# Kernel tuning notes

Hardware: AMD Instinct MI355X
Metric: run time of the kernel (lower is better)

Reference implementation:

```python
import jax, jax.numpy as jnp
import numpy as np

B, T, IN, H, OUT = 4096, 365, 32, 256, 1


def setup_inputs() -> dict:
    key = jax.random.key(0)
    ks = jax.random.split(key, 6)
    s_ih = 1.0 / np.sqrt(H)
    return {
        "xd": jax.random.normal(ks[0], (B, T, IN), dtype=jnp.float32),
        "w_ih": jax.random.uniform(ks[1], (4 * H, IN), minval=-s_ih, maxval=s_ih, dtype=jnp.float32),
        "w_hh": jax.random.uniform(ks[2], (4 * H, H), minval=-s_ih, maxval=s_ih, dtype=jnp.float32),
        "b": jax.random.uniform(ks[3], (4 * H,), minval=-s_ih, maxval=s_ih, dtype=jnp.float32),
        "w_out": jax.random.uniform(ks[4], (OUT, H), minval=-s_ih, maxval=s_ih, dtype=jnp.float32),
        "b_out": jax.random.uniform(ks[5], (OUT,), minval=-s_ih, maxval=s_ih, dtype=jnp.float32),
    }


def reference(xd, w_ih, w_hh, b, w_out, b_out):
    # xd: [B, T, IN]. Scan LSTM cell over time; gate order i, f, g, o (equinox/torch).
    Bsz = xd.shape[0]
    Hs = w_hh.shape[1]
    xs = jnp.swapaxes(xd, 0, 1)  # [T, B, IN]
    # Precompute input projections for all timesteps (same math, one big GEMM).
    x_proj = jnp.einsum("tbi,gi->tbg", xs, w_ih) + b  # [T, B, 4H]

    def step(state, xp):
        h, c = state  # [B, H] each
        gates = xp + h @ w_hh.T  # [B, 4H]
        i, f, g, o = jnp.split(gates, 4, axis=-1)
        i = jax.nn.sigmoid(i)
        f = jax.nn.sigmoid(f)
        g = jnp.tanh(g)
        o = jax.nn.sigmoid(o)
        c = f * c + i * g
        h = o * jnp.tanh(c)
        return (h, c), None

    init = (jnp.zeros((Bsz, Hs), xd.dtype), jnp.zeros((Bsz, Hs), xd.dtype))
    (h_T, _), _ = jax.lax.scan(step, init, x_proj)
    return jax.nn.relu(h_T @ w_out.T + b_out)  # [B, OUT]
```

## Files before the change

kernel.cpp:

```cpp
#include <hip/hip_runtime.h>
#include <hip/hip_fp16.h>

#define T_SZ 365
#define IN_SZ 32
#define H_SZ 256
#define G4 1024
#define K_SZ 288
#define M_BLK 32
#define NGRP 128
#define NTHR 512
#define NBLK 256
#define XPB 80
#define HROWB 512
#define HS_BYTES (M_BLK * HROWB)

#define ARR_OFF (640*1024)
#define HX_OFF  (1024*1024)

typedef _Float16 f16x8 __attribute__((ext_vector_type(8)));
typedef _Float16 f16x2 __attribute__((ext_vector_type(2)));
typedef float f32x4 __attribute__((ext_vector_type(4)));
typedef unsigned long long u64;

__device__ __forceinline__ float fast_sigmoid(float x) {
    float e = __builtin_amdgcn_exp2f(-1.4426950408889634f * x);
    return __builtin_amdgcn_rcpf(1.0f + e);
}
__device__ __forceinline__ float fast_tanh(float x) {
    float e = __builtin_amdgcn_exp2f(2.8853900817779268f * x);
    return 1.0f - 2.0f * __builtin_amdgcn_rcpf(1.0f + e);
}

__global__ void pack_w_kernel(const float* __restrict__ w_ih,
                              const float* __restrict__ w_hh,
                              _Float16* __restrict__ wp) {
    int idx = blockIdx.x * 256 + threadIdx.x;
    if (idx >= G4 * K_SZ) return;
    int g = idx / K_SZ, k = idx - g * K_SZ;
    float v = (k < H_SZ) ? w_hh[g * H_SZ + k] : w_ih[g * IN_SZ + (k - H_SZ)];
    wp[idx] = (_Float16)v;
}

__global__ void init_sync_kernel(unsigned int* arrive) {
    for (int i = threadIdx.x; i < NGRP * 2 * 16; i += 256) arrive[i] = 0u;
}

__global__ __launch_bounds__(NTHR, 2) void lstm_kernel(
    const float* __restrict__ xd, const float* __restrict__ b,
    const _Float16* __restrict__ wp, const float* __restrict__ w_out,
    const float* __restrict__ b_out, float* __restrict__ out,
    u64* hx, unsigned int* arrive)
{
    __shared__ __align__(16) char hsb[2 * HS_BYTES];
    __shared__ __align__(16) char x_s[M_BLK * XPB];

    const int tid  = threadIdx.x;
    const int wq   = tid >> 6;
    const int lane = tid & 63;
    const int quad = lane >> 4;
    const int l16  = lane & 15;
    const int blk  = blockIdx.x;
    const int g    = blk & (NGRP - 1);
    const int q    = blk >> 7;

    const int jcol = q * 128 + wq * 16 + l16;

    f16x8 wfr[4][9];
#pragma unroll
    for (int G = 0; G < 4; ++G) {
        const _Float16* wr = wp + (size_t)(G * 256 + jcol) * K_SZ + quad * 8;
#pragma unroll
        for (int kt = 0; kt < 9; ++kt)
            wfr[G][kt] = *(const f16x8*)(wr + kt * 32);
    }
    float bias[4];
#pragma unroll
    for (int G = 0; G < 4; ++G) bias[G] = b[G * 256 + jcol];

    const int swz_l = (l16 & 7) << 4;
    int a_off[8];
#pragma unroll
    for (int kt = 0; kt < 8; ++kt)
        a_off[kt] = l16 * HROWB + ((kt * 64 + quad * 16) ^ swz_l);
    const int x_off = l16 * XPB + quad * 16;

    const int xr = tid >> 4;
    const int xe = tid & 15;
    const int xs_byte = xr * XPB + xe * 4;
    const float* xrow = xd + (size_t)(g * M_BLK + xr) * (T_SZ * IN_SZ) + xe * 2;
    float2 xa = *(const float2*)xrow;

    const int pr  = tid >> 5;
    const int pw  = tid & 31;
    const int swz_p = (pr & 7) << 4;
    const int push_l0 = pr * HROWB + ((q * 256 + pw * 8) ^ swz_p);
    const int pull_l0 = pr * HROWB + (((1 - q) * 256 + pw * 8) ^ swz_p);
    const int push_u0 = q * 1024 + tid;
    const int pull_u0 = (1 - q) * 1024 + tid;

    {
        u64* z = (u64*)hsb;
#pragma unroll
        for (int i = 0; i < 4; ++i) z[tid * 4 + i] = 0ull;
    }
    *(f16x2*)(x_s + xs_byte) = (f16x2){(_Float16)xa.x, (_Float16)xa.y};

    f32x4 creg[2];
    creg[0] = (f32x4){0.f, 0.f, 0.f, 0.f};
    creg[1] = (f32x4){0.f, 0.f, 0.f, 0.f};

    __syncthreads();

    unsigned int* myf = &arrive[(g * 2 + q) * 16];
    unsigned int* prf = &arrive[(g * 2 + (1 - q)) * 16];
    const f32x4 vzero = {0.f, 0.f, 0.f, 0.f};

    int pb = 0;
    for (int t = 0; t < T_SZ; ++t) {
        const char* hsR = hsb + pb * HS_BYTES;
        char* hsW = hsb + (pb ^ 1) * HS_BYTES;

        f32x4 acc[2][4];
#pragma unroll
        for (int mt = 0; mt < 2; ++mt)
#pragma unroll
            for (int G = 0; G < 4; ++G) acc[mt][G] = vzero;

#pragma unroll
        for (int kt = 0; kt < 8; ++kt) {
            f16x8 a0 = *(const f16x8*)(hsR + a_off[kt]);
            f16x8 a1 = *(const f16x8*)(hsR + a_off[kt] + 16 * HROWB);
#pragma unroll
            for (int G = 0; G < 4; ++G) {
                acc[0][G] = __builtin_amdgcn_mfma_f32_16x16x32_f16(a0, wfr[G][kt], acc[0][G], 0, 0, 0);
                acc[1][G] = __builtin_amdgcn_mfma_f32_16x16x32_f16(a1, wfr[G][kt], acc[1][G], 0, 0, 0);
            }
        }
        {
            f16x8 a0 = *(const f16x8*)(x_s + x_off);
            f16x8 a1 = *(const f16x8*)(x_s + x_off + 16 * XPB);
#pragma unroll
            for (int G = 0; G < 4; ++G) {
                acc[0][G] = __builtin_amdgcn_mfma_f32_16x16x32_f16(a0, wfr[G][8], acc[0][G], 0, 0, 0);
                acc[1][G] = __builtin_amdgcn_mfma_f32_16x16x32_f16(a1, wfr[G][8], acc[1][G], 0, 0, 0);
            }
        }

#pragma unroll
        for (int mt = 0; mt < 2; ++mt) {
#pragma unroll
            for (int r = 0; r < 4; ++r) {
                float iv = fast_sigmoid(acc[mt][0][r] + bias[0]);
                float fv = fast_sigmoid(acc[mt][1][r] + bias[1]);
                float gv = fast_tanh  (acc[mt][2][r] + bias[2]);
                float ov = fast_sigmoid(acc[mt][3][r] + bias[3]);
                float cv = fv * creg[mt][r] + iv * gv;
                creg[mt][r] = cv;
                float hv = ov * fast_tanh(cv);
                int m = mt * 16 + quad * 4 + r;
                *(_Float16*)(hsW + m * HROWB + ((jcol * 2) ^ ((m & 7) << 4))) = (_Float16)hv;
            }
        }
        asm volatile("s_waitcnt lgkmcnt(0)" ::: "memory");
        __builtin_amdgcn_s_barrier();

        u64* hxg = hx + ((size_t)pb * NGRP + g) * 2048;
        {
            u64 p0 = *(const u64*)(hsW + push_l0);
            u64 p1 = *(const u64*)(hsW + push_l0 + 16 * HROWB);
            __hip_atomic_store(&hxg[push_u0],       p0, __ATOMIC_RELAXED, __HIP_MEMORY_SCOPE_AGENT);
            __hip_atomic_store(&hxg[push_u0 + 512], p1, __ATOMIC_RELAXED, __HIP_MEMORY_SCOPE_AGENT);
        }
        if (t + 1 < T_SZ) {
            xa = *(const float2*)(xrow + (size_t)(t + 1) * IN_SZ);
            asm volatile("s_waitcnt vmcnt(1)" ::: "memory");
        } else {
            asm volatile("s_waitcnt vmcnt(0)" ::: "memory");
        }
        __builtin_amdgcn_s_barrier();

        if (tid == 0) {
            __hip_atomic_store(myf, (unsigned int)(t + 1),
                               __ATOMIC_RELAXED, __HIP_MEMORY_SCOPE_AGENT);
            while (__hip_atomic_load(prf, __ATOMIC_RELAXED, __HIP_MEMORY_SCOPE_AGENT) < (unsigned int)(t + 1))
                __builtin_amdgcn_s_sleep(1);
        }
        __builtin_amdgcn_s_barrier();
        asm volatile("" ::: "memory");

        {
            u64 v0 = __hip_atomic_load(&hxg[pull_u0],       __ATOMIC_RELAXED, __HIP_MEMORY_SCOPE_AGENT);
            u64 v1 = __hip_atomic_load(&hxg[pull_u0 + 512], __ATOMIC_RELAXED, __HIP_MEMORY_SCOPE_AGENT);
            *(u64*)(hsW + pull_l0)              = v0;
            *(u64*)(hsW + pull_l0 + 16 * HROWB) = v1;
        }
        if (t + 1 < T_SZ)
            *(f16x2*)(x_s + xs_byte) = (f16x2){(_Float16)xa.x, (_Float16)xa.y};
        asm volatile("s_waitcnt lgkmcnt(0)" ::: "memory");
        __builtin_amdgcn_s_barrier();
        pb ^= 1;
    }

    if (q == 0) {
        const char* hsF = hsb + pb * HS_BYTES;
        const int m = tid >> 4, p = tid & 15;
        const int swzm = (m & 7) << 4;
        float sum = 0.f;
#pragma unroll
        for (int jj = 0; jj < 16; ++jj) {
            int j = p * 16 + jj;
            sum += (float)*(const _Float16*)(hsF + m * HROWB + ((j * 2) ^ swzm)) * w_out[j];
        }
        sum += __shfl_xor(sum, 1);
        sum += __shfl_xor(sum, 2);
        sum += __shfl_xor(sum, 4);
        sum += __shfl_xor(sum, 8);
        if (p == 0) out[(size_t)g * M_BLK + m] = fmaxf(sum + b_out[0], 0.f);
    }
}

extern "C" void kernel_launch(void* const* d_in, const int* in_sizes, int n_in,
                              void* d_out, int out_size, void* d_ws, size_t ws_size,
                              hipStream_t stream) {
    const float* xd    = (const float*)d_in[0];
    const float* w_ih  = (const float*)d_in[1];
    const float* w_hh  = (const float*)d_in[2];
    const float* b     = (const float*)d_in[3];
    const float* w_out = (const float*)d_in[4];
    const float* b_out = (const float*)d_in[5];
    float* out = (float*)d_out;

    _Float16* wp = (_Float16*)d_ws;
    unsigned int* arrive = (unsigned int*)((char*)d_ws + ARR_OFF);
    u64* hx = (u64*)((char*)d_ws + HX_OFF);

    pack_w_kernel<<<(G4 * K_SZ + 255) / 256, 256, 0, stream>>>(w_ih, w_hh, wp);
    init_sync_kernel<<<1, 256, 0, stream>>>(arrive);
    lstm_kernel<<<NBLK, NTHR, 0, stream>>>(xd, b, wp, w_out, b_out, out, hx, arrive);
}
```

Baseline: 1.608 ms.

## Overlap cross-block h exchange with local-half recurrent GEMM via split-K pipelining

Splits the recurrent K dimension into the block's own hidden half and the partner block's half. The own-half MFMAs (plus the x-projection tile) for the next step are issued before and after the inter-block flag wait, and the partner's h values stay in registers until the next step. This hides spin-wait and global-load latency behind tensor work and drops one barrier per step. It also prefetches x two steps ahead, at the cost of more live registers and more complex hand-written waitcnt ordering.

```diff
diff --git a/kernel.cpp b/kernel.cpp
--- a/kernel.cpp
+++ b/kernel.cpp
@@ -45,6 +45,19 @@
     for (int i = threadIdx.x; i < NGRP * 2 * 16; i += 256) arrive[i] = 0u;
 }
 
+#define GEMM_TILE(base, off, stride, slot) do {                                            \
+    f16x8 a0_ = *(const f16x8*)((const char*)(base) + (off));                              \
+    f16x8 a1_ = *(const f16x8*)((const char*)(base) + (off) + 16 * (stride));              \
+    acc[0][0] = __builtin_amdgcn_mfma_f32_16x16x32_f16(a0_, wfr[0][slot], acc[0][0],0,0,0);\
+    acc[1][0] = __builtin_amdgcn_mfma_f32_16x16x32_f16(a1_, wfr[0][slot], acc[1][0],0,0,0);\
+    acc[0][1] = __builtin_amdgcn_mfma_f32_16x16x32_f16(a0_, wfr[1][slot], acc[0][1],0,0,0);\
+    acc[1][1] = __builtin_amdgcn_mfma_f32_16x16x32_f16(a1_, wfr[1][slot], acc[1][1],0,0,0);\
+    acc[0][2] = __builtin_amdgcn_mfma_f32_16x16x32_f16(a0_, wfr[2][slot], acc[0][2],0,0,0);\
+    acc[1][2] = __builtin_amdgcn_mfma_f32_16x16x32_f16(a1_, wfr[2][slot], acc[1][2],0,0,0);\
+    acc[0][3] = __builtin_amdgcn_mfma_f32_16x16x32_f16(a0_, wfr[3][slot], acc[0][3],0,0,0);\
+    acc[1][3] = __builtin_amdgcn_mfma_f32_16x16x32_f16(a1_, wfr[3][slot], acc[1][3],0,0,0);\
+} while (0)
+
 __global__ __launch_bounds__(NTHR, 2) void lstm_kernel(
     const float* __restrict__ xd, const float* __restrict__ b,
     const _Float16* __restrict__ wp, const float* __restrict__ w_out,
@@ -64,6 +77,8 @@
     const int q    = blk >> 7;
 
     const int jcol = q * 128 + wq * 16 + l16;
+    const int ktO  = q * 4;
+    const int ktP  = (1 - q) * 4;
 
     f16x8 wfr[4][9];
 #pragma unroll
@@ -88,7 +103,6 @@
     const int xe = tid & 15;
     const int xs_byte = xr * XPB + xe * 4;
     const float* xrow = xd + (size_t)(g * M_BLK + xr) * (T_SZ * IN_SZ) + xe * 2;
-    float2 xa = *(const float2*)xrow;
 
     const int pr  = tid >> 5;
     const int pw  = tid & 31;
@@ -103,7 +117,11 @@
 #pragma unroll
         for (int i = 0; i < 4; ++i) z[tid * 4 + i] = 0ull;
     }
-    *(f16x2*)(x_s + xs_byte) = (f16x2){(_Float16)xa.x, (_Float16)xa.y};
+    {
+        float2 x0 = *(const float2*)xrow;
+        *(f16x2*)(x_s + xs_byte) = (f16x2){(_Float16)x0.x, (_Float16)x0.y};
+    }
+    float2 xa = *(const float2*)(xrow + IN_SZ);
 
     f32x4 creg[2];
     creg[0] = (f32x4){0.f, 0.f, 0.f, 0.f};
@@ -115,36 +133,34 @@
     unsigned int* prf = &arrive[(g * 2 + (1 - q)) * 16];
     const f32x4 vzero = {0.f, 0.f, 0.f, 0.f};
 
+    f32x4 acc[2][4];
+#pragma unroll
+    for (int mt = 0; mt < 2; ++mt)
+#pragma unroll
+        for (int G = 0; G < 4; ++G) acc[mt][G] = vzero;
+    GEMM_TILE(x_s, x_off, XPB, 8);
+#pragma unroll
+    for (int kt = 0; kt < 4; ++kt)
+        GEMM_TILE(hsb, a_off[ktO + kt], HROWB, ktO + kt);
+
+    u64 pv0 = 0, pv1 = 0;
     int pb = 0;
     for (int t = 0; t < T_SZ; ++t) {
-        const char* hsR = hsb + pb * HS_BYTES;
-        char* hsW = hsb + (pb ^ 1) * HS_BYTES;
-
-        f32x4 acc[2][4];
-#pragma unroll
-        for (int mt = 0; mt < 2; ++mt)
-#pragma unroll
-            for (int G = 0; G < 4; ++G) acc[mt][G] = vzero;
-
-#pragma unroll
-        for (int kt = 0; kt < 8; ++kt) {
-            f16x8 a0 = *(const f16x8*)(hsR + a_off[kt]);
-            f16x8 a1 = *(const f16x8*)(hsR + a_off[kt] + 16 * HROWB);
-#pragma unroll
-            for (int G = 0; G < 4; ++G) {
-                acc[0][G] = __builtin_amdgcn_mfma_f32_16x16x32_f16(a0, wfr[G][kt], acc[0][G], 0, 0, 0);
-                acc[1][G] = __builtin_amdgcn_mfma_f32_16x16x32_f16(a1, wfr[G][kt], acc[1][G], 0, 0, 0);
-            }
-        }
-        {
-            f16x8 a0 = *(const f16x8*)(x_s + x_off);
-            f16x8 a1 = *(const f16x8*)(x_s + x_off + 16 * XPB);
-#pragma unroll
-            for (int G = 0; G < 4; ++G) {
-                acc[0][G] = __builtin_amdgcn_mfma_f32_16x16x32_f16(a0, wfr[G][8], acc[0][G], 0, 0, 0);
-                acc[1][G] = __builtin_amdgcn_mfma_f32_16x16x32_f16(a1, wfr[G][8], acc[1][G], 0, 0, 0);
-            }
-        }
+        char* hsCur = hsb + pb * HS_BYTES;
+        char* hsNxt = hsb + (pb ^ 1) * HS_BYTES;
+        u64* hxg = hx + ((size_t)(pb ^ 1) * NGRP + g) * 2048;
+
+        if (t > 0) {
+            asm volatile("s_waitcnt vmcnt(0)" ::: "memory");
+            *(u64*)(hsCur + pull_l0)              = pv0;
+            *(u64*)(hsCur + pull_l0 + 16 * HROWB) = pv1;
+        }
+        asm volatile("s_waitcnt lgkmcnt(0)" ::: "memory");
+        __builtin_amdgcn_s_barrier();
+
+#pragma unroll
+        for (int kt = 0; kt < 4; ++kt)
+            GEMM_TILE(hsCur, a_off[ktP + kt], HROWB, ktP + kt);
 
 #pragma unroll
         for (int mt = 0; mt < 2; ++mt) {
@@ -158,27 +174,38 @@
                 creg[mt][r] = cv;
                 float hv = ov * fast_tanh(cv);
                 int m = mt * 16 + quad * 4 + r;
-                *(_Float16*)(hsW + m * HROWB + ((jcol * 2) ^ ((m & 7) << 4))) = (_Float16)hv;
+                *(_Float16*)(hsNxt + m * HROWB + ((jcol * 2) ^ ((m & 7) << 4))) = (_Float16)hv;
             }
         }
+        if (t + 1 < T_SZ)
+            *(f16x2*)(x_s + xs_byte) = (f16x2){(_Float16)xa.x, (_Float16)xa.y};
         asm volatile("s_waitcnt lgkmcnt(0)" ::: "memory");
         __builtin_amdgcn_s_barrier();
 
-        u64* hxg = hx + ((size_t)pb * NGRP + g) * 2048;
         {
-            u64 p0 = *(const u64*)(hsW + push_l0);
-            u64 p1 = *(const u64*)(hsW + push_l0 + 16 * HROWB);
+            u64 p0 = *(const u64*)(hsNxt + push_l0);
+            u64 p1 = *(const u64*)(hsNxt + push_l0 + 16 * HROWB);
             __hip_atomic_store(&hxg[push_u0],       p0, __ATOMIC_RELAXED, __HIP_MEMORY_SCOPE_AGENT);
             __hip_atomic_store(&hxg[push_u0 + 512], p1, __ATOMIC_RELAXED, __HIP_MEMORY_SCOPE_AGENT);
         }
-        if (t + 1 < T_SZ) {
-            xa = *(const float2*)(xrow + (size_t)(t + 1) * IN_SZ);
-            asm volatile("s_waitcnt vmcnt(1)" ::: "memory");
-        } else {
-            asm volatile("s_waitcnt vmcnt(0)" ::: "memory");
-        }
-        __builtin_amdgcn_s_barrier();
-
+        asm volatile("" ::: "memory");
+        {
+            int tn = (t + 2 < T_SZ) ? t + 2 : T_SZ - 1;
+            xa = *(const float2*)(xrow + (size_t)tn * IN_SZ);
+        }
+
+        const bool more = (t + 1 < T_SZ);
+        if (more) {
+#pragma unroll
+            for (int mt = 0; mt < 2; ++mt)
+#pragma unroll
+                for (int G = 0; G < 4; ++G) acc[mt][G] = vzero;
+            GEMM_TILE(x_s, x_off, XPB, 8);
+            GEMM_TILE(hsNxt, a_off[ktO + 0], HROWB, ktO + 0);
+            GEMM_TILE(hsNxt, a_off[ktO + 1], HROWB, ktO + 1);
+        }
+
+        asm volatile("s_waitcnt vmcnt(1)" ::: "memory");
         if (tid == 0) {
             __hip_atomic_store(myf, (unsigned int)(t + 1),
                                __ATOMIC_RELAXED, __HIP_MEMORY_SCOPE_AGENT);
@@ -186,19 +213,24 @@
                 __builtin_amdgcn_s_sleep(1);
         }
         __builtin_amdgcn_s_barrier();
-        asm volatile("" ::: "memory");
-
-        {
-            u64 v0 = __hip_atomic_load(&hxg[pull_u0],       __ATOMIC_RELAXED, __HIP_MEMORY_SCOPE_AGENT);
-            u64 v1 = __hip_atomic_load(&hxg[pull_u0 + 512], __ATOMIC_RELAXED, __HIP_MEMORY_SCOPE_AGENT);
-            *(u64*)(hsW + pull_l0)              = v0;
-            *(u64*)(hsW + pull_l0 + 16 * HROWB) = v1;
-        }
-        if (t + 1 < T_SZ)
-            *(f16x2*)(x_s + xs_byte) = (f16x2){(_Float16)xa.x, (_Float16)xa.y};
+
+        pv0 = __hip_atomic_load(&hxg[pull_u0],       __ATOMIC_RELAXED, __HIP_MEMORY_SCOPE_AGENT);
+        pv1 = __hip_atomic_load(&hxg[pull_u0 + 512], __ATOMIC_RELAXED, __HIP_MEMORY_SCOPE_AGENT);
+
+        if (more) {
+            GEMM_TILE(hsNxt, a_off[ktO + 2], HROWB, ktO + 2);
+            GEMM_TILE(hsNxt, a_off[ktO + 3], HROWB, ktO + 3);
+        }
+        pb ^= 1;
+    }
+
+    {
+        char* hsF = hsb + pb * HS_BYTES;
+        asm volatile("s_waitcnt vmcnt(0)" ::: "memory");
+        *(u64*)(hsF + pull_l0)              = pv0;
+        *(u64*)(hsF + pull_l0 + 16 * HROWB) = pv1;
         asm volatile("s_waitcnt lgkmcnt(0)" ::: "memory");
         __builtin_amdgcn_s_barrier();
-        pb ^= 1;
     }
 
     if (q == 0) {
```

After: 4.427 ms. 175% more time.

## Split batch tile into two slabs to overlap cross-block exchange with compute

Applied to the files above, without the earlier changes.

The 32-row batch tile is split into two 16-row slabs, each with its own hidden-state buffers, arrival flags and exchange region. Slab B's GEMM and activations now run while slab A's half of h from the partner block is in flight, and the reverse. The aim is to hide the global-memory handshake latency that was fully exposed on every timestep. In exchange it adds a second flag handshake and more barriers per step, and the per-slab MFMA chains are shorter, which gives less independent work to cover MFMA latency.

```diff
diff --git a/kernel.cpp b/kernel.cpp
--- a/kernel.cpp
+++ b/kernel.cpp
@@ -7,12 +7,14 @@
 #define G4 1024
 #define K_SZ 288
 #define M_BLK 32
+#define M_SLAB 16
 #define NGRP 128
 #define NTHR 512
 #define NBLK 256
 #define XPB 80
 #define HROWB 512
-#define HS_BYTES (M_BLK * HROWB)
+#define HSLAB (M_SLAB * HROWB)
+#define HXG 1024
 
 #define ARR_OFF (640*1024)
 #define HX_OFF  (1024*1024)
@@ -42,8 +44,39 @@
 }
 
 __global__ void init_sync_kernel(unsigned int* arrive) {
-    for (int i = threadIdx.x; i < NGRP * 2 * 16; i += 256) arrive[i] = 0u;
-}
+    for (int i = threadIdx.x; i < NGRP * 4 * 16; i += 256) arrive[i] = 0u;
+}
+
+#define GEMM_SLAB(acc, hbase, xoff) do {                                                    \
+    _Pragma("unroll")                                                                       \
+    for (int kt_ = 0; kt_ < 8; ++kt_) {                                                     \
+        f16x8 a_ = *(const f16x8*)((const char*)(hbase) + a_off[kt_]);                      \
+        _Pragma("unroll")                                                                   \
+        for (int G_ = 0; G_ < 4; ++G_)                                                      \
+            acc[G_] = __builtin_amdgcn_mfma_f32_16x16x32_f16(a_, wfr[G_][kt_], acc[G_],0,0,0);\
+    }                                                                                       \
+    {                                                                                       \
+        f16x8 a_ = *(const f16x8*)(x_s + (xoff));                                           \
+        _Pragma("unroll")                                                                   \
+        for (int G_ = 0; G_ < 4; ++G_)                                                      \
+            acc[G_] = __builtin_amdgcn_mfma_f32_16x16x32_f16(a_, wfr[G_][8], acc[G_],0,0,0);\
+    }                                                                                       \
+} while (0)
+
+#define ACT_STORE(acc, creg, hdst) do {                                                     \
+    _Pragma("unroll")                                                                       \
+    for (int r_ = 0; r_ < 4; ++r_) {                                                        \
+        float iv = fast_sigmoid(acc[0][r_] + bias[0]);                                      \
+        float fv = fast_sigmoid(acc[1][r_] + bias[1]);                                      \
+        float gv = fast_tanh  (acc[2][r_] + bias[2]);                                       \
+        float ov = fast_sigmoid(acc[3][r_] + bias[3]);                                      \
+        float cv = fv * creg[r_] + iv * gv;                                                 \
+        creg[r_] = cv;                                                                      \
+        float hv = ov * fast_tanh(cv);                                                      \
+        int m_ = quad * 4 + r_;                                                             \
+        *(_Float16*)((hdst) + m_ * HROWB + ((jcol * 2) ^ ((m_ & 7) << 4))) = (_Float16)hv;  \
+    }                                                                                       \
+} while (0)
 
 __global__ __launch_bounds__(NTHR, 2) void lstm_kernel(
     const float* __restrict__ xd, const float* __restrict__ b,
@@ -51,7 +84,8 @@
     const float* __restrict__ b_out, float* __restrict__ out,
     u64* hx, unsigned int* arrive)
 {
-    __shared__ __align__(16) char hsb[2 * HS_BYTES];
+    __shared__ __align__(16) char hsA[2][HSLAB];
+    __shared__ __align__(16) char hsB[2][HSLAB];
     __shared__ __align__(16) char x_s[M_BLK * XPB];
 
     const int tid  = threadIdx.x;
@@ -82,134 +116,123 @@
 #pragma unroll
     for (int kt = 0; kt < 8; ++kt)
         a_off[kt] = l16 * HROWB + ((kt * 64 + quad * 16) ^ swz_l);
-    const int x_off = l16 * XPB + quad * 16;
+    const int x_offA = l16 * XPB + quad * 16;
+    const int x_offB = x_offA + M_SLAB * XPB;
 
     const int xr = tid >> 4;
     const int xe = tid & 15;
     const int xs_byte = xr * XPB + xe * 4;
     const float* xrow = xd + (size_t)(g * M_BLK + xr) * (T_SZ * IN_SZ) + xe * 2;
-    float2 xa = *(const float2*)xrow;
-
-    const int pr  = tid >> 5;
-    const int pw  = tid & 31;
-    const int swz_p = (pr & 7) << 4;
-    const int push_l0 = pr * HROWB + ((q * 256 + pw * 8) ^ swz_p);
-    const int pull_l0 = pr * HROWB + (((1 - q) * 256 + pw * 8) ^ swz_p);
-    const int push_u0 = q * 1024 + tid;
-    const int pull_u0 = (1 - q) * 1024 + tid;
+
+    const int prow = lane >> 2;
+    const int pch  = lane & 3;
+    const int push_lb = prow * HROWB + ((q * 256 + wq * 32 + pch * 8) ^ ((prow & 7) << 4));
+    const int push_u  = q * 512 + wq * 64 + lane;
+    const int pwv = tid >> 6, prw = (tid & 63) >> 2, pcc = tid & 3;
+    const int pull_u  = (1 - q) * 512 + tid;
+    const int pull_lb = prw * HROWB + (((1 - q) * 256 + pwv * 32 + pcc * 8) ^ ((prw & 7) << 4));
 
     {
-        u64* z = (u64*)hsb;
-#pragma unroll
-        for (int i = 0; i < 4; ++i) z[tid * 4 + i] = 0ull;
-    }
-    *(f16x2*)(x_s + xs_byte) = (f16x2){(_Float16)xa.x, (_Float16)xa.y};
-
-    f32x4 creg[2];
-    creg[0] = (f32x4){0.f, 0.f, 0.f, 0.f};
-    creg[1] = (f32x4){0.f, 0.f, 0.f, 0.f};
+        u64* zA = (u64*)&hsA[0][0];
+        u64* zB = (u64*)&hsB[0][0];
+        zA[tid] = 0ull; zA[tid + 512] = 0ull;
+        zB[tid] = 0ull; zB[tid + 512] = 0ull;
+    }
+    {
+        float2 x0 = *(const float2*)xrow;
+        *(f16x2*)(x_s + xs_byte) = (f16x2){(_Float16)x0.x, (_Float16)x0.y};
+    }
+
+    f32x4 cregA = (f32x4){0.f, 0.f, 0.f, 0.f};
+    f32x4 cregB = (f32x4){0.f, 0.f, 0.f, 0.f};
+    const f32x4 vzero = {0.f, 0.f, 0.f, 0.f};
 
     __syncthreads();
 
-    unsigned int* myf = &arrive[(g * 2 + q) * 16];
-    unsigned int* prf = &arrive[(g * 2 + (1 - q)) * 16];
-    const f32x4 vzero = {0.f, 0.f, 0.f, 0.f};
-
+    unsigned int* myfA = &arrive[(g * 4 + q * 2 + 0) * 16];
+    unsigned int* prfA = &arrive[(g * 4 + (1 - q) * 2 + 0) * 16];
+    unsigned int* myfB = myfA + 16;
+    unsigned int* prfB = prfA + 16;
+
+    float2 xa = {0.f, 0.f};
+    u64 pvb = 0;
     int pb = 0;
+
     for (int t = 0; t < T_SZ; ++t) {
-        const char* hsR = hsb + pb * HS_BYTES;
-        char* hsW = hsb + (pb ^ 1) * HS_BYTES;
-
-        f32x4 acc[2][4];
-#pragma unroll
-        for (int mt = 0; mt < 2; ++mt)
-#pragma unroll
-            for (int G = 0; G < 4; ++G) acc[mt][G] = vzero;
-
-#pragma unroll
-        for (int kt = 0; kt < 8; ++kt) {
-            f16x8 a0 = *(const f16x8*)(hsR + a_off[kt]);
-            f16x8 a1 = *(const f16x8*)(hsR + a_off[kt] + 16 * HROWB);
-#pragma unroll
-            for (int G = 0; G < 4; ++G) {
-                acc[0][G] = __builtin_amdgcn_mfma_f32_16x16x32_f16(a0, wfr[G][kt], acc[0][G], 0, 0, 0);
-                acc[1][G] = __builtin_amdgcn_mfma_f32_16x16x32_f16(a1, wfr[G][kt], acc[1][G], 0, 0, 0);
-            }
-        }
+        char* hsA_R = hsA[pb];     char* hsA_W = hsA[pb ^ 1];
+        char* hsB_R = hsB[pb];     char* hsB_W = hsB[pb ^ 1];
+        u64* hxA = hx + ((size_t)(((pb ^ 1) << 1) + 0) * NGRP + g) * HXG;
+        u64* hxB = hx + ((size_t)(((pb ^ 1) << 1) + 1) * NGRP + g) * HXG;
+
+        f32x4 accA[4];
+#pragma unroll
+        for (int G = 0; G < 4; ++G) accA[G] = vzero;
+        GEMM_SLAB(accA, hsA_R, x_offA);
+        ACT_STORE(accA, cregA, hsA_W);
+        asm volatile("s_waitcnt lgkmcnt(0)" ::: "memory");
         {
-            f16x8 a0 = *(const f16x8*)(x_s + x_off);
-            f16x8 a1 = *(const f16x8*)(x_s + x_off + 16 * XPB);
-#pragma unroll
-            for (int G = 0; G < 4; ++G) {
-                acc[0][G] = __builtin_amdgcn_mfma_f32_16x16x32_f16(a0, wfr[G][8], acc[0][G], 0, 0, 0);
-                acc[1][G] = __builtin_amdgcn_mfma_f32_16x16x32_f16(a1, wfr[G][8], acc[1][G], 0, 0, 0);
-            }
-        }
-
-#pragma unroll
-        for (int mt = 0; mt < 2; ++mt) {
-#pragma unroll
-            for (int r = 0; r < 4; ++r) {
-                float iv = fast_sigmoid(acc[mt][0][r] + bias[0]);
-                float fv = fast_sigmoid(acc[mt][1][r] + bias[1]);
-                float gv = fast_tanh  (acc[mt][2][r] + bias[2]);
-                float ov = fast_sigmoid(acc[mt][3][r] + bias[3]);
-                float cv = fv * creg[mt][r] + iv * gv;
-                creg[mt][r] = cv;
-                float hv = ov * fast_tanh(cv);
-                int m = mt * 16 + quad * 4 + r;
-                *(_Float16*)(hsW + m * HROWB + ((jcol * 2) ^ ((m & 7) << 4))) = (_Float16)hv;
-            }
-        }
-        asm volatile("s_waitcnt lgkmcnt(0)" ::: "memory");
-        __builtin_amdgcn_s_barrier();
-
-        u64* hxg = hx + ((size_t)pb * NGRP + g) * 2048;
+            u64 pa = *(const u64*)(hsA_W + push_lb);
+            __hip_atomic_store(&hxA[push_u], pa, __ATOMIC_RELAXED, __HIP_MEMORY_SCOPE_AGENT);
+        }
         {
-            u64 p0 = *(const u64*)(hsW + push_l0);
-            u64 p1 = *(const u64*)(hsW + push_l0 + 16 * HROWB);
-            __hip_atomic_store(&hxg[push_u0],       p0, __ATOMIC_RELAXED, __HIP_MEMORY_SCOPE_AGENT);
-            __hip_atomic_store(&hxg[push_u0 + 512], p1, __ATOMIC_RELAXED, __HIP_MEMORY_SCOPE_AGENT);
-        }
-        if (t + 1 < T_SZ) {
-            xa = *(const float2*)(xrow + (size_t)(t + 1) * IN_SZ);
-            asm volatile("s_waitcnt vmcnt(1)" ::: "memory");
-        } else {
-            asm volatile("s_waitcnt vmcnt(0)" ::: "memory");
-        }
-        __builtin_amdgcn_s_barrier();
-
+            int tn = (t + 1 < T_SZ) ? t + 1 : T_SZ - 1;
+            xa = *(const float2*)(xrow + (size_t)tn * IN_SZ);
+        }
+        asm volatile("s_waitcnt vmcnt(1)" ::: "memory");
+        if (t > 0)
+            *(u64*)(hsB_R + pull_lb) = pvb;
+        asm volatile("s_waitcnt lgkmcnt(0)" ::: "memory");
+        __builtin_amdgcn_s_barrier();
         if (tid == 0) {
-            __hip_atomic_store(myf, (unsigned int)(t + 1),
-                               __ATOMIC_RELAXED, __HIP_MEMORY_SCOPE_AGENT);
-            while (__hip_atomic_load(prf, __ATOMIC_RELAXED, __HIP_MEMORY_SCOPE_AGENT) < (unsigned int)(t + 1))
+            __hip_atomic_store(myfA, (unsigned int)(t + 1), __ATOMIC_RELAXED, __HIP_MEMORY_SCOPE_AGENT);
+            while (__hip_atomic_load(prfA, __ATOMIC_RELAXED, __HIP_MEMORY_SCOPE_AGENT) < (unsigned int)(t + 1))
                 __builtin_amdgcn_s_sleep(1);
         }
         __builtin_amdgcn_s_barrier();
-        asm volatile("" ::: "memory");
-
+        u64 pva = __hip_atomic_load(&hxA[pull_u], __ATOMIC_RELAXED, __HIP_MEMORY_SCOPE_AGENT);
+
+        f32x4 accB[4];
+#pragma unroll
+        for (int G = 0; G < 4; ++G) accB[G] = vzero;
+        GEMM_SLAB(accB, hsB_R, x_offB);
+        ACT_STORE(accB, cregB, hsB_W);
+        asm volatile("s_waitcnt lgkmcnt(0)" ::: "memory");
         {
-            u64 v0 = __hip_atomic_load(&hxg[pull_u0],       __ATOMIC_RELAXED, __HIP_MEMORY_SCOPE_AGENT);
-            u64 v1 = __hip_atomic_load(&hxg[pull_u0 + 512], __ATOMIC_RELAXED, __HIP_MEMORY_SCOPE_AGENT);
-            *(u64*)(hsW + pull_l0)              = v0;
-            *(u64*)(hsW + pull_l0 + 16 * HROWB) = v1;
-        }
+            u64 pbv = *(const u64*)(hsB_W + push_lb);
+            __hip_atomic_store(&hxB[push_u], pbv, __ATOMIC_RELAXED, __HIP_MEMORY_SCOPE_AGENT);
+        }
+
+        asm volatile("s_waitcnt vmcnt(0)" ::: "memory");
+        *(u64*)(hsA_W + pull_lb) = pva;
+        asm volatile("s_waitcnt lgkmcnt(0)" ::: "memory");
+        __builtin_amdgcn_s_barrier();
         if (t + 1 < T_SZ)
             *(f16x2*)(x_s + xs_byte) = (f16x2){(_Float16)xa.x, (_Float16)xa.y};
-        asm volatile("s_waitcnt lgkmcnt(0)" ::: "memory");
-        __builtin_amdgcn_s_barrier();
+        if (tid == 0) {
+            __hip_atomic_store(myfB, (unsigned int)(t + 1), __ATOMIC_RELAXED, __HIP_MEMORY_SCOPE_AGENT);
+            while (__hip_atomic_load(prfB, __ATOMIC_RELAXED, __HIP_MEMORY_SCOPE_AGENT) < (unsigned int)(t + 1))
+                __builtin_amdgcn_s_sleep(1);
+        }
+        asm volatile("s_waitcnt lgkmcnt(0)" ::: "memory");
+        __builtin_amdgcn_s_barrier();
+        pvb = __hip_atomic_load(&hxB[pull_u], __ATOMIC_RELAXED, __HIP_MEMORY_SCOPE_AGENT);
         pb ^= 1;
     }
 
+    asm volatile("s_waitcnt vmcnt(0)" ::: "memory");
+    *(u64*)(hsB[pb] + pull_lb) = pvb;
+    asm volatile("s_waitcnt lgkmcnt(0)" ::: "memory");
+    __builtin_amdgcn_s_barrier();
+
     if (q == 0) {
-        const char* hsF = hsb + pb * HS_BYTES;
         const int m = tid >> 4, p = tid & 15;
+        const char* hsF = (m < M_SLAB ? hsA[pb] : hsB[pb]) + (m & 15) * HROWB;
         const int swzm = (m & 7) << 4;
         float sum = 0.f;
 #pragma unroll
         for (int jj = 0; jj < 16; ++jj) {
             int j = p * 16 + jj;
-            sum += (float)*(const _Float16*)(hsF + m * HROWB + ((j * 2) ^ swzm)) * w_out[j];
+            sum += (float)*(const _Float16*)(hsF + ((j * 2) ^ swzm)) * w_out[j];
         }
         sum += __shfl_xor(sum, 1);
         sum += __shfl_xor(sum, 2);
```

Measured after the change: 1.784 ms. 1.11x slower.
